# Performance work log

Hardware: AMD Instinct MI355X
Metric: run time of the kernel (lower is better)

## Reference

```python
import jax, jax.numpy as jnp
import numpy as np

HID = 128  # hidden_dim

def _run_layer(x, W, b):
    """x: [B,T,Cin,H,W]; W: [4*HID, Cin+HID] (gate order i,f,o,g); b: [4*HID]."""
    B, T, Cin, H, Wd = x.shape
    h0 = jnp.zeros((B, HID, H, Wd), x.dtype)
    c0 = jnp.zeros_like(h0)
    xt = jnp.moveaxis(x, 1, 0)  # [T,B,Cin,H,W]

    def step(carry, x_t):
        h, c = carry
        z = jnp.concatenate([x_t, h], axis=1)                     # [B,Cin+HID,H,W]
        gates = jnp.einsum('bchw,gc->bghw', z, W) + b[None, :, None, None]
        i, f, o, g = jnp.split(gates, 4, axis=1)                  # each [B,HID,H,W]
        c_n = jax.nn.sigmoid(f) * c + jax.nn.sigmoid(i) * jnp.tanh(g)
        h_n = jax.nn.sigmoid(o) * jnp.tanh(c_n)
        return (h_n, c_n), h_n

    (hT, cT), hs = jax.lax.scan(step, (h0, c0), xt)
    return jnp.moveaxis(hs, 0, 1), hT, cT  # [B,T,HID,H,W], [B,HID,H,W] x2


def setup_inputs() -> dict:
    key = jax.random.key(0)
    ks = jax.random.split(key, 5)
    B, T, Cin, H, W = 8, 32, 64, 32, 32
    x = jax.random.normal(ks[0], (B, T, Cin, H, W), dtype=jnp.float32)
    W0 = jax.random.normal(ks[1], (4 * HID, Cin + HID), dtype=jnp.float32) * 0.05
    b0 = jax.random.normal(ks[2], (4 * HID,), dtype=jnp.float32) * 0.05
    W1 = jax.random.normal(ks[3], (4 * HID, HID + HID), dtype=jnp.float32) * 0.05
    b1 = jax.random.normal(ks[4], (4 * HID,), dtype=jnp.float32) * 0.05
    return {"x": x, "W0": W0, "b0": b0, "W1": W1, "b1": b1}


def reference(x, W0, b0, W1, b1):
    y0, _, _ = _run_layer(x, W0, b0)      # layer 0
    y1, hT, cT = _run_layer(y0, W1, b1)   # layer 1 (last layer)
    return y1, hT, cT
```

## Files before the change

kernel.cpp:

```cpp
#include <hip/hip_runtime.h>

typedef short bf16x8 __attribute__((ext_vector_type(8)));
typedef short bf16x4 __attribute__((ext_vector_type(4)));
typedef float f32x4  __attribute__((ext_vector_type(4)));

#define HID 128
#define TT 32
#define HWSZ 1024
#define PX 32
#define NTHREADS 512

__device__ __forceinline__ float bf2f(unsigned short u) {
    union { unsigned int i; float f; } v; v.i = ((unsigned int)u) << 16; return v.f;
}
__device__ __forceinline__ unsigned short f2bf(float f) {
    union { float f; unsigned int i; } v; v.f = f;
    unsigned int u = v.i;
    return (unsigned short)((u + 0x7fffu + ((u >> 16) & 1u)) >> 16);
}
__device__ __forceinline__ float frcp(float x) { return __builtin_amdgcn_rcpf(x); }
__device__ __forceinline__ float sigm(float x) { return frcp(1.0f + __expf(-x)); }
__device__ __forceinline__ float ftanh(float x){ return 1.0f - 2.0f * frcp(1.0f + __expf(2.0f * x)); }

template <int CIN, bool FINAL, bool IN_LOCAL, bool OUT_LOCAL>
__global__ __launch_bounds__(NTHREADS, 2)
void lstm_layer(const void* __restrict__ in_, const float* __restrict__ W,
                const float* __restrict__ bias, void* __restrict__ y_,
                float* __restrict__ hT, float* __restrict__ cT)
{
    constexpr int K      = CIN + HID;
    constexpr int XK     = CIN / 32;
    constexpr int KITERS = K / 32;
    constexpr int XB0 = 0, XB1 = CIN, HB0 = 2 * CIN, HB1 = 2 * CIN + HID;
    constexpr int PITCH = 2 * CIN + 2 * HID + 8;
    constexpr int NIT = (PX * CIN / 4) / NTHREADS;

    const float* inF          = (const float*)in_;
    const unsigned short* inL = (const unsigned short*)in_;
    float* yF                 = (float*)y_;
    unsigned short* yL        = (unsigned short*)y_;

    __shared__ __align__(16) unsigned short z[PX][PITCH];

    const int tid  = threadIdx.x;
    const int wave = tid >> 6;
    const int lane = tid & 63;
    const int q    = lane >> 4;
    const int ln   = lane & 15;

    const int p0  = blockIdx.x * PX;
    const int b   = p0 >> 10;
    const int hw0 = p0 & 1023;

    const long long locbase = (long long)blockIdx.x * TT * PX * HID;
    const long long inFbase = (long long)b * TT * CIN * HWSZ + hw0;

    bf16x8 Af[KITERS][4];
    #pragma unroll
    for (int k = 0; k < KITERS; ++k) {
        #pragma unroll
        for (int g = 0; g < 4; ++g) {
            const float* wp = W + (g * HID + wave * 16 + ln) * K + k * 32 + q * 8;
            bf16x8 v;
            #pragma unroll
            for (int j = 0; j < 8; ++j) v[j] = (short)f2bf(wp[j]);
            Af[k][g] = v;
        }
    }
    f32x4 bs[4];
    #pragma unroll
    for (int g = 0; g < 4; ++g)
        bs[g] = *(const f32x4*)(bias + g * HID + wave * 16 + q * 4);

    const int ch0 = wave * 16 + q * 4;

    #pragma unroll
    for (int idx = tid; idx < PX * HID; idx += NTHREADS)
        z[idx & (PX - 1)][HB0 + (idx >> 5)] = 0;
    if (IN_LOCAL) {
        bf16x8 v = *(const bf16x8*)(inL + locbase + tid * 8);
        *(bf16x8*)&z[tid >> 4][XB0 + (tid & 15) * 8] = v;
    } else {
        #pragma unroll
        for (int it = 0; it < NIT; ++it) {
            const int idx = tid + it * NTHREADS;
            const int px = idx & 31, c0 = (idx >> 5) * 4;
            bf16x4 v;
            #pragma unroll
            for (int j = 0; j < 4; ++j) v[j] = (short)f2bf(inF[inFbase + (c0 + j) * HWSZ + px]);
            *(bf16x4*)&z[px][XB0 + c0] = v;
        }
    }
    __syncthreads();

    float cst[2][4];
    #pragma unroll
    for (int mt = 0; mt < 2; ++mt)
        #pragma unroll
        for (int r = 0; r < 4; ++r) cst[mt][r] = 0.0f;

    #pragma unroll 2
    for (int t = 0; t < TT; ++t) {
        const int cur = t & 1;
        const int xb_r = cur ? XB1 : XB0, xb_w = cur ? XB0 : XB1;
        const int hb_r = cur ? HB1 : HB0, hb_w = cur ? HB0 : HB1;
        const int tn = (t + 1 < TT) ? (t + 1) : t;

        bf16x8 pfv;
        float pff[NIT][4];
        if (IN_LOCAL) {
            pfv = *(const bf16x8*)(inL + locbase + (long long)tn * PX * HID + tid * 8);
        } else {
            #pragma unroll
            for (int it = 0; it < NIT; ++it) {
                const int idx = tid + it * NTHREADS;
                const int px = idx & 31, c0 = (idx >> 5) * 4;
                #pragma unroll
                for (int j = 0; j < 4; ++j)
                    pff[it][j] = inF[inFbase + (long long)tn * CIN * HWSZ + (c0 + j) * HWSZ + px];
            }
        }

        f32x4 acc[2][4];
        #pragma unroll
        for (int mt = 0; mt < 2; ++mt)
            #pragma unroll
            for (int g = 0; g < 4; ++g) acc[mt][g] = (f32x4){0.f, 0.f, 0.f, 0.f};

        #pragma unroll
        for (int k = 0; k < KITERS; ++k) {
            const int koff = (k < XK) ? (xb_r + k * 32) : (hb_r + (k - XK) * 32);
            const bf16x8 p0v = *(const bf16x8*)&z[ln][koff + q * 8];
            const bf16x8 p1v = *(const bf16x8*)&z[16 + ln][koff + q * 8];
            #pragma unroll
            for (int g = 0; g < 4; ++g) {
                acc[0][g] = __builtin_amdgcn_mfma_f32_16x16x32_bf16(Af[k][g], p0v, acc[0][g], 0, 0, 0);
                acc[1][g] = __builtin_amdgcn_mfma_f32_16x16x32_bf16(Af[k][g], p1v, acc[1][g], 0, 0, 0);
            }
        }

        #pragma unroll
        for (int mt = 0; mt < 2; ++mt) {
            const int px = mt * 16 + ln;
            bf16x4 hv;
            #pragma unroll
            for (int r = 0; r < 4; ++r) {
                const float iv = sigm(acc[mt][0][r] + bs[0][r]);
                const float fv = sigm(acc[mt][1][r] + bs[1][r]);
                const float ov = sigm(acc[mt][2][r] + bs[2][r]);
                const float gv = ftanh(acc[mt][3][r] + bs[3][r]);
                const float c  = fv * cst[mt][r] + iv * gv;
                cst[mt][r] = c;
                const float h = ov * ftanh(c);
                hv[r] = (short)f2bf(h);
                if (FINAL && t == TT - 1)
                    cT[(b * HID + ch0 + r) * HWSZ + hw0 + px] = c;
            }
            *(bf16x4*)&z[px][hb_w + ch0] = hv;
        }

        if (IN_LOCAL) {
            *(bf16x8*)&z[tid >> 4][xb_w + (tid & 15) * 8] = pfv;
        } else {
            #pragma unroll
            for (int it = 0; it < NIT; ++it) {
                const int idx = tid + it * NTHREADS;
                const int px = idx & 31, c0 = (idx >> 5) * 4;
                bf16x4 v;
                #pragma unroll
                for (int j = 0; j < 4; ++j) v[j] = (short)f2bf(pff[it][j]);
                *(bf16x4*)&z[px][xb_w + c0] = v;
            }
        }

        __syncthreads();

        if (FINAL || !OUT_LOCAL) {
            const int c = tid >> 2, px8 = (tid & 3) * 8;
            float f[8];
            #pragma unroll
            for (int j = 0; j < 8; ++j) f[j] = bf2f(z[px8 + j][hb_w + c]);
            float* yp = yF + (long long)(b * TT + t) * HID * HWSZ + c * HWSZ + hw0 + px8;
            *(f32x4*)yp       = (f32x4){f[0], f[1], f[2], f[3]};
            *(f32x4*)(yp + 4) = (f32x4){f[4], f[5], f[6], f[7]};
            if (FINAL && t == TT - 1) {
                float* hp = hT + (long long)(b * HID + c) * HWSZ + hw0 + px8;
                *(f32x4*)hp       = (f32x4){f[0], f[1], f[2], f[3]};
                *(f32x4*)(hp + 4) = (f32x4){f[4], f[5], f[6], f[7]};
            }
        } else {
            bf16x8 v = *(const bf16x8*)&z[tid >> 4][hb_w + (tid & 15) * 8];
            *(bf16x8*)(yL + locbase + (long long)t * PX * HID + tid * 8) = v;
        }
    }
}

extern "C" void kernel_launch(void* const* d_in, const int* in_sizes, int n_in,
                              void* d_out, int out_size, void* d_ws, size_t ws_size,
                              hipStream_t stream) {
    const float* x  = (const float*)d_in[0];
    const float* W0 = (const float*)d_in[1];
    const float* b0 = (const float*)d_in[2];
    const float* W1 = (const float*)d_in[3];
    const float* b1 = (const float*)d_in[4];
    float* out = (float*)d_out;

    float* y  = out;
    float* hT = out + 33554432;
    float* cT = out + 34603008;

    dim3 grid(8192 / PX), block(NTHREADS);

    const size_t y0_bytes = (size_t)8 * HWSZ * TT * HID * 2;
    if (ws_size >= y0_bytes) {
        unsigned short* y0 = (unsigned short*)d_ws;
        lstm_layer<64,  false, false, true ><<<grid, block, 0, stream>>>(x,  W0, b0, y0, nullptr, nullptr);
        lstm_layer<128, true,  true,  false><<<grid, block, 0, stream>>>(y0, W1, b1, y,  hT, cT);
    } else {
        lstm_layer<64,  false, false, false><<<grid, block, 0, stream>>>(x, W0, b0, y, nullptr, nullptr);
        lstm_layer<128, true,  false, false><<<grid, block, 0, stream>>>(y, W1, b1, y, hT, cT);
    }
}
```

Before: 355.3 us.

## Software-pipeline input projection one step ahead and write y directly from registers

Restructures the recurrent loop so the input-to-gate MFMA for step t+1 runs during step t, after the recurrent h MFMAs. This takes the x-part of the GEMM off the serial dependency chain. A three-slot x ring buffer in LDS with prefetch two steps ahead supports this, and the bias is folded into the accumulator init. The fp32 y/hT outputs are now stored straight from registers instead of going through an LDS round trip after the barrier. The change also uses the v_cvt_pk_bf16_f32 instruction for packed conversion and replaces __syncthreads with a raw s_barrier, at the cost of more accumulator registers and less coalesced 4-byte strided global stores.

```diff
diff --git a/kernel.cpp b/kernel.cpp
--- a/kernel.cpp
+++ b/kernel.cpp
@@ -3,6 +3,7 @@
 typedef short bf16x8 __attribute__((ext_vector_type(8)));
 typedef short bf16x4 __attribute__((ext_vector_type(4)));
 typedef float f32x4  __attribute__((ext_vector_type(4)));
+typedef unsigned int u32x2 __attribute__((ext_vector_type(2)));
 
 #define HID 128
 #define TT 32
@@ -10,13 +11,15 @@
 #define PX 32
 #define NTHREADS 512
 
-__device__ __forceinline__ float bf2f(unsigned short u) {
-    union { unsigned int i; float f; } v; v.i = ((unsigned int)u) << 16; return v.f;
-}
 __device__ __forceinline__ unsigned short f2bf(float f) {
     union { float f; unsigned int i; } v; v.f = f;
     unsigned int u = v.i;
     return (unsigned short)((u + 0x7fffu + ((u >> 16) & 1u)) >> 16);
+}
+__device__ __forceinline__ unsigned int cvt_pk_bf16(float lo, float hi) {
+    unsigned int r;
+    asm("v_cvt_pk_bf16_f32 %0, %1, %2" : "=v"(r) : "v"(lo), "v"(hi));
+    return r;
 }
 __device__ __forceinline__ float frcp(float x) { return __builtin_amdgcn_rcpf(x); }
 __device__ __forceinline__ float sigm(float x) { return frcp(1.0f + __expf(-x)); }
@@ -30,9 +33,10 @@
 {
     constexpr int K      = CIN + HID;
     constexpr int XK     = CIN / 32;
+    constexpr int HK     = HID / 32;
     constexpr int KITERS = K / 32;
-    constexpr int XB0 = 0, XB1 = CIN, HB0 = 2 * CIN, HB1 = 2 * CIN + HID;
-    constexpr int PITCH = 2 * CIN + 2 * HID + 8;
+    constexpr int HB0 = 3 * CIN, HB1 = 3 * CIN + HID;
+    constexpr int PITCH = 3 * CIN + 2 * HID + 8;
     constexpr int NIT = (PX * CIN / 4) / NTHREADS;
 
     const float* inF          = (const float*)in_;
@@ -73,22 +77,31 @@
         bs[g] = *(const f32x4*)(bias + g * HID + wave * 16 + q * 4);
 
     const int ch0 = wave * 16 + q * 4;
+    float* const ybase = yF + ((long long)b * TT * HID + ch0) * HWSZ + hw0;
 
     #pragma unroll
     for (int idx = tid; idx < PX * HID; idx += NTHREADS)
         z[idx & (PX - 1)][HB0 + (idx >> 5)] = 0;
     if (IN_LOCAL) {
-        bf16x8 v = *(const bf16x8*)(inL + locbase + tid * 8);
-        *(bf16x8*)&z[tid >> 4][XB0 + (tid & 15) * 8] = v;
+        bf16x8 v0 = *(const bf16x8*)(inL + locbase + tid * 8);
+        bf16x8 v1 = *(const bf16x8*)(inL + locbase + (long long)PX * HID + tid * 8);
+        *(bf16x8*)&z[tid >> 4][(tid & 15) * 8] = v0;
+        *(bf16x8*)&z[tid >> 4][CIN + (tid & 15) * 8] = v1;
     } else {
         #pragma unroll
         for (int it = 0; it < NIT; ++it) {
             const int idx = tid + it * NTHREADS;
-            const int px = idx & 31, c0 = (idx >> 5) * 4;
-            bf16x4 v;
+            const int pxs = idx & 31, c0 = (idx >> 5) * 4;
+            float a0[4], a1[4];
             #pragma unroll
-            for (int j = 0; j < 4; ++j) v[j] = (short)f2bf(inF[inFbase + (c0 + j) * HWSZ + px]);
-            *(bf16x4*)&z[px][XB0 + c0] = v;
+            for (int j = 0; j < 4; ++j) a0[j] = inF[inFbase + (c0 + j) * HWSZ + pxs];
+            #pragma unroll
+            for (int j = 0; j < 4; ++j) a1[j] = inF[inFbase + (long long)CIN * HWSZ + (c0 + j) * HWSZ + pxs];
+            u32x2 v0, v1;
+            v0[0] = cvt_pk_bf16(a0[0], a0[1]); v0[1] = cvt_pk_bf16(a0[2], a0[3]);
+            v1[0] = cvt_pk_bf16(a1[0], a1[1]); v1[1] = cvt_pk_bf16(a1[2], a1[3]);
+            *(u32x2*)&z[pxs][c0] = v0;
+            *(u32x2*)&z[pxs][CIN + c0] = v1;
         }
     }
     __syncthreads();
@@ -99,100 +112,121 @@
         #pragma unroll
         for (int r = 0; r < 4; ++r) cst[mt][r] = 0.0f;
 
-    #pragma unroll 2
-    for (int t = 0; t < TT; ++t) {
-        const int cur = t & 1;
-        const int xb_r = cur ? XB1 : XB0, xb_w = cur ? XB0 : XB1;
-        const int hb_r = cur ? HB1 : HB0, hb_w = cur ? HB0 : HB1;
-        const int tn = (t + 1 < TT) ? (t + 1) : t;
-
-        bf16x8 pfv;
-        float pff[NIT][4];
-        if (IN_LOCAL) {
-            pfv = *(const bf16x8*)(inL + locbase + (long long)tn * PX * HID + tid * 8);
-        } else {
-            #pragma unroll
-            for (int it = 0; it < NIT; ++it) {
-                const int idx = tid + it * NTHREADS;
-                const int px = idx & 31, c0 = (idx >> 5) * 4;
-                #pragma unroll
-                for (int j = 0; j < 4; ++j)
-                    pff[it][j] = inF[inFbase + (long long)tn * CIN * HWSZ + (c0 + j) * HWSZ + px];
-            }
+    f32x4 accA[2][4], accB[2][4];
+    #pragma unroll
+    for (int g = 0; g < 4; ++g) { accA[0][g] = bs[g]; accA[1][g] = bs[g]; }
+    #pragma unroll
+    for (int k = 0; k < XK; ++k) {
+        const int koff = k * 32;
+        const bf16x8 pv0 = *(const bf16x8*)&z[ln][koff + q * 8];
+        const bf16x8 pv1 = *(const bf16x8*)&z[16 + ln][koff + q * 8];
+        #pragma unroll
+        for (int g = 0; g < 4; ++g) {
+            accA[0][g] = __builtin_amdgcn_mfma_f32_16x16x32_bf16(Af[k][g], pv0, accA[0][g], 0, 0, 0);
+            accA[1][g] = __builtin_amdgcn_mfma_f32_16x16x32_bf16(Af[k][g], pv1, accA[1][g], 0, 0, 0);
         }
-
-        f32x4 acc[2][4];
-        #pragma unroll
-        for (int mt = 0; mt < 2; ++mt)
-            #pragma unroll
-            for (int g = 0; g < 4; ++g) acc[mt][g] = (f32x4){0.f, 0.f, 0.f, 0.f};
-
-        #pragma unroll
-        for (int k = 0; k < KITERS; ++k) {
-            const int koff = (k < XK) ? (xb_r + k * 32) : (hb_r + (k - XK) * 32);
-            const bf16x8 p0v = *(const bf16x8*)&z[ln][koff + q * 8];
-            const bf16x8 p1v = *(const bf16x8*)&z[16 + ln][koff + q * 8];
-            #pragma unroll
-            for (int g = 0; g < 4; ++g) {
-                acc[0][g] = __builtin_amdgcn_mfma_f32_16x16x32_bf16(Af[k][g], p0v, acc[0][g], 0, 0, 0);
-                acc[1][g] = __builtin_amdgcn_mfma_f32_16x16x32_bf16(Af[k][g], p1v, acc[1][g], 0, 0, 0);
-            }
-        }
-
-        #pragma unroll
-        for (int mt = 0; mt < 2; ++mt) {
-            const int px = mt * 16 + ln;
-            bf16x4 hv;
-            #pragma unroll
-            for (int r = 0; r < 4; ++r) {
-                const float iv = sigm(acc[mt][0][r] + bs[0][r]);
-                const float fv = sigm(acc[mt][1][r] + bs[1][r]);
-                const float ov = sigm(acc[mt][2][r] + bs[2][r]);
-                const float gv = ftanh(acc[mt][3][r] + bs[3][r]);
-                const float c  = fv * cst[mt][r] + iv * gv;
-                cst[mt][r] = c;
-                const float h = ov * ftanh(c);
-                hv[r] = (short)f2bf(h);
-                if (FINAL && t == TT - 1)
-                    cT[(b * HID + ch0 + r) * HWSZ + hw0 + px] = c;
-            }
-            *(bf16x4*)&z[px][hb_w + ch0] = hv;
-        }
-
-        if (IN_LOCAL) {
-            *(bf16x8*)&z[tid >> 4][xb_w + (tid & 15) * 8] = pfv;
-        } else {
-            #pragma unroll
-            for (int it = 0; it < NIT; ++it) {
-                const int idx = tid + it * NTHREADS;
-                const int px = idx & 31, c0 = (idx >> 5) * 4;
-                bf16x4 v;
-                #pragma unroll
-                for (int j = 0; j < 4; ++j) v[j] = (short)f2bf(pff[it][j]);
-                *(bf16x4*)&z[px][xb_w + c0] = v;
-            }
-        }
-
-        __syncthreads();
-
-        if (FINAL || !OUT_LOCAL) {
-            const int c = tid >> 2, px8 = (tid & 3) * 8;
-            float f[8];
-            #pragma unroll
-            for (int j = 0; j < 8; ++j) f[j] = bf2f(z[px8 + j][hb_w + c]);
-            float* yp = yF + (long long)(b * TT + t) * HID * HWSZ + c * HWSZ + hw0 + px8;
-            *(f32x4*)yp       = (f32x4){f[0], f[1], f[2], f[3]};
-            *(f32x4*)(yp + 4) = (f32x4){f[4], f[5], f[6], f[7]};
-            if (FINAL && t == TT - 1) {
-                float* hp = hT + (long long)(b * HID + c) * HWSZ + hw0 + px8;
-                *(f32x4*)hp       = (f32x4){f[0], f[1], f[2], f[3]};
-                *(f32x4*)(hp + 4) = (f32x4){f[4], f[5], f[6], f[7]};
-            }
-        } else {
-            bf16x8 v = *(const bf16x8*)&z[tid >> 4][hb_w + (tid & 15) * 8];
-            *(bf16x8*)(yL + locbase + (long long)t * PX * HID + tid * 8) = v;
-        }
-    }
+    }
+
+#define LSTM_STEP(T, PAR, ACCC, ACCN)                                            \
+    {                                                                            \
+        const int hb_r = (PAR) ? HB1 : HB0;                                      \
+        const int hb_w = (PAR) ? HB0 : HB1;                                      \
+        const int xs_n = ((T) + 1) % 3;                                          \
+        const int xs_w = ((T) + 2) % 3;                                          \
+        const int tn2  = ((T) + 2 < TT) ? (T) + 2 : TT - 1;                      \
+        bf16x8 pfv; float pff[NIT][4];                                           \
+        if (IN_LOCAL) {                                                          \
+            pfv = *(const bf16x8*)(inL + locbase + (long long)tn2 * PX * HID + tid * 8); \
+        } else {                                                                 \
+            _Pragma("unroll")                                                    \
+            for (int it = 0; it < NIT; ++it) {                                   \
+                const int idx = tid + it * NTHREADS;                             \
+                const int pxs = idx & 31, c0 = (idx >> 5) * 4;                   \
+                _Pragma("unroll")                                                \
+                for (int j = 0; j < 4; ++j)                                      \
+                    pff[it][j] = inF[inFbase + (long long)tn2 * CIN * HWSZ + (c0 + j) * HWSZ + pxs]; \
+            }                                                                    \
+        }                                                                        \
+        _Pragma("unroll")                                                        \
+        for (int k = 0; k < HK; ++k) {                                           \
+            const int koff = hb_r + k * 32;                                      \
+            const bf16x8 pv0 = *(const bf16x8*)&z[ln][koff + q * 8];             \
+            const bf16x8 pv1 = *(const bf16x8*)&z[16 + ln][koff + q * 8];        \
+            _Pragma("unroll")                                                    \
+            for (int g = 0; g < 4; ++g) {                                        \
+                ACCC[0][g] = __builtin_amdgcn_mfma_f32_16x16x32_bf16(Af[XK + k][g], pv0, ACCC[0][g], 0, 0, 0); \
+                ACCC[1][g] = __builtin_amdgcn_mfma_f32_16x16x32_bf16(Af[XK + k][g], pv1, ACCC[1][g], 0, 0, 0); \
+            }                                                                    \
+        }                                                                        \
+        _Pragma("unroll")                                                        \
+        for (int g = 0; g < 4; ++g) { ACCN[0][g] = bs[g]; ACCN[1][g] = bs[g]; }  \
+        _Pragma("unroll")                                                        \
+        for (int k = 0; k < XK; ++k) {                                           \
+            const int koff = xs_n * CIN + k * 32;                                \
+            const bf16x8 pv0 = *(const bf16x8*)&z[ln][koff + q * 8];             \
+            const bf16x8 pv1 = *(const bf16x8*)&z[16 + ln][koff + q * 8];        \
+            _Pragma("unroll")                                                    \
+            for (int g = 0; g < 4; ++g) {                                        \
+                ACCN[0][g] = __builtin_amdgcn_mfma_f32_16x16x32_bf16(Af[k][g], pv0, ACCN[0][g], 0, 0, 0); \
+                ACCN[1][g] = __builtin_amdgcn_mfma_f32_16x16x32_bf16(Af[k][g], pv1, ACCN[1][g], 0, 0, 0); \
+            }                                                                    \
+        }                                                                        \
+        _Pragma("unroll")                                                        \
+        for (int mt = 0; mt < 2; ++mt) {                                         \
+            const int px = mt * 16 + ln;                                         \
+            float hr[4];                                                         \
+            _Pragma("unroll")                                                    \
+            for (int r = 0; r < 4; ++r) {                                        \
+                const float iv = sigm(ACCC[mt][0][r]);                           \
+                const float fv = sigm(ACCC[mt][1][r]);                           \
+                const float ov = sigm(ACCC[mt][2][r]);                           \
+                const float gv = ftanh(ACCC[mt][3][r]);                          \
+                const float c  = fv * cst[mt][r] + iv * gv;                      \
+                cst[mt][r] = c;                                                  \
+                hr[r] = ov * ftanh(c);                                           \
+                if (FINAL && (T) == TT - 1)                                      \
+                    cT[((long long)(b * HID + ch0 + r)) * HWSZ + hw0 + px] = c;  \
+            }                                                                    \
+            u32x2 hv;                                                            \
+            hv[0] = cvt_pk_bf16(hr[0], hr[1]);                                   \
+            hv[1] = cvt_pk_bf16(hr[2], hr[3]);                                   \
+            *(u32x2*)&z[px][hb_w + ch0] = hv;                                    \
+            if (FINAL || !OUT_LOCAL) {                                           \
+                float* yp = ybase + (long long)(T) * (HID * HWSZ) + px;          \
+                yp[0] = hr[0]; yp[HWSZ] = hr[1];                                 \
+                yp[2 * HWSZ] = hr[2]; yp[3 * HWSZ] = hr[3];                      \
+                if (FINAL && (T) == TT - 1) {                                    \
+                    float* hp = hT + ((long long)(b * HID + ch0)) * HWSZ + hw0 + px; \
+                    hp[0] = hr[0]; hp[HWSZ] = hr[1];                             \
+                    hp[2 * HWSZ] = hr[2]; hp[3 * HWSZ] = hr[3];                  \
+                }                                                                \
+            }                                                                    \
+        }                                                                        \
+        if (IN_LOCAL) {                                                          \
+            *(bf16x8*)&z[tid >> 4][xs_w * CIN + (tid & 15) * 8] = pfv;           \
+        } else {                                                                 \
+            _Pragma("unroll")                                                    \
+            for (int it = 0; it < NIT; ++it) {                                   \
+                const int idx = tid + it * NTHREADS;                             \
+                const int pxs = idx & 31, c0 = (idx >> 5) * 4;                   \
+                u32x2 xv;                                                        \
+                xv[0] = cvt_pk_bf16(pff[it][0], pff[it][1]);                     \
+                xv[1] = cvt_pk_bf16(pff[it][2], pff[it][3]);                     \
+                *(u32x2*)&z[pxs][xs_w * CIN + c0] = xv;                          \
+            }                                                                    \
+        }                                                                        \
+        asm volatile("s_waitcnt lgkmcnt(0)\n\ts_barrier" ::: "memory");          \
+        if (!FINAL && OUT_LOCAL) {                                               \
+            bf16x8 hv8 = *(const bf16x8*)&z[tid >> 4][hb_w + (tid & 15) * 8];    \
+            *(bf16x8*)(yL + locbase + (long long)(T) * PX * HID + tid * 8) = hv8; \
+        }                                                                        \
+    }
+
+    for (int t = 0; t < TT; t += 2) {
+        LSTM_STEP(t,     0, accA, accB)
+        LSTM_STEP(t + 1, 1, accB, accA)
+    }
+#undef LSTM_STEP
 }
 
 extern "C" void kernel_launch(void* const* d_in, const int* in_sizes, int n_in,
```

New measurement: 364.6 us. 2.6% more time.

## Split LSTM block into input-projection and recurrent warp groups with LDS handoff

Applied to the files above, without the earlier changes.

Doubles the block to 1024 threads. Eight waves compute the input projection W_x·x_{t+1} plus bias one step ahead and hand it off through LDS accumulators, while the other eight waves do only the recurrent W_h·h GEMM and the gate math. This takes the input GEMM and the global x prefetch off the serial critical path of the recurrence. Other changes: output is written directly from registers without a transposing LDS pass, LDS reads use XOR swizzling, and bf16 packing uses v_cvt_pk_bf16_f32. The cost is two barriers per step across 16 waves, plus an fp32 accumulator exchange through LDS, with added risk to occupancy and register pressure.

```diff
diff --git a/kernel.cpp b/kernel.cpp
--- a/kernel.cpp
+++ b/kernel.cpp
@@ -1,52 +1,58 @@
 #include <hip/hip_runtime.h>
 
 typedef short bf16x8 __attribute__((ext_vector_type(8)));
-typedef short bf16x4 __attribute__((ext_vector_type(4)));
 typedef float f32x4  __attribute__((ext_vector_type(4)));
+typedef unsigned int u32x2 __attribute__((ext_vector_type(2)));
 
 #define HID 128
 #define TT 32
 #define HWSZ 1024
 #define PX 32
-#define NTHREADS 512
-
-__device__ __forceinline__ float bf2f(unsigned short u) {
-    union { unsigned int i; float f; } v; v.i = ((unsigned int)u) << 16; return v.f;
-}
+#define NTHREADS 1024
+
 __device__ __forceinline__ unsigned short f2bf(float f) {
     union { float f; unsigned int i; } v; v.f = f;
     unsigned int u = v.i;
     return (unsigned short)((u + 0x7fffu + ((u >> 16) & 1u)) >> 16);
 }
+__device__ __forceinline__ unsigned int cvt_pk_bf16(float lo, float hi) {
+    unsigned int r;
+    asm("v_cvt_pk_bf16_f32 %0, %1, %2" : "=v"(r) : "v"(lo), "v"(hi));
+    return r;
+}
 __device__ __forceinline__ float frcp(float x) { return __builtin_amdgcn_rcpf(x); }
 __device__ __forceinline__ float sigm(float x) { return frcp(1.0f + __expf(-x)); }
 __device__ __forceinline__ float ftanh(float x){ return 1.0f - 2.0f * frcp(1.0f + __expf(2.0f * x)); }
 
+#define BAR() asm volatile("s_waitcnt lgkmcnt(0)\n\ts_barrier" ::: "memory")
+
 template <int CIN, bool FINAL, bool IN_LOCAL, bool OUT_LOCAL>
-__global__ __launch_bounds__(NTHREADS, 2)
+__global__ __launch_bounds__(NTHREADS, 4)
 void lstm_layer(const void* __restrict__ in_, const float* __restrict__ W,
                 const float* __restrict__ bias, void* __restrict__ y_,
                 float* __restrict__ hT, float* __restrict__ cT)
 {
-    constexpr int K      = CIN + HID;
-    constexpr int XK     = CIN / 32;
-    constexpr int KITERS = K / 32;
-    constexpr int XB0 = 0, XB1 = CIN, HB0 = 2 * CIN, HB1 = 2 * CIN + HID;
-    constexpr int PITCH = 2 * CIN + 2 * HID + 8;
-    constexpr int NIT = (PX * CIN / 4) / NTHREADS;
+    constexpr int XK  = CIN / 32;
+    constexpr int HK  = HID / 32;
+    constexpr int NIT = (PX * CIN / 4) / 512;
 
     const float* inF          = (const float*)in_;
     const unsigned short* inL = (const unsigned short*)in_;
     float* yF                 = (float*)y_;
     unsigned short* yL        = (unsigned short*)y_;
 
-    __shared__ __align__(16) unsigned short z[PX][PITCH];
+    __shared__ __align__(16) float          accS[8 * 2 * 4 * 256];
+    __shared__ __align__(16) unsigned short hS[2][PX][HID];
+    __shared__ __align__(16) unsigned short xS[2][PX][CIN];
+    __shared__ __align__(16) float          biasS[4 * HID];
 
     const int tid  = threadIdx.x;
     const int wave = tid >> 6;
     const int lane = tid & 63;
     const int q    = lane >> 4;
     const int ln   = lane & 15;
+    const bool isB = wave < 8;
+    const int  wp  = wave & 7;
 
     const int p0  = blockIdx.x * PX;
     const int b   = p0 >> 10;
@@ -55,142 +61,217 @@
     const long long locbase = (long long)blockIdx.x * TT * PX * HID;
     const long long inFbase = (long long)b * TT * CIN * HWSZ + hw0;
 
-    bf16x8 Af[KITERS][4];
-    #pragma unroll
-    for (int k = 0; k < KITERS; ++k) {
-        #pragma unroll
-        for (int g = 0; g < 4; ++g) {
-            const float* wp = W + (g * HID + wave * 16 + ln) * K + k * 32 + q * 8;
-            bf16x8 v;
-            #pragma unroll
-            for (int j = 0; j < 8; ++j) v[j] = (short)f2bf(wp[j]);
-            Af[k][g] = v;
-        }
-    }
-    f32x4 bs[4];
-    #pragma unroll
-    for (int g = 0; g < 4; ++g)
-        bs[g] = *(const f32x4*)(bias + g * HID + wave * 16 + q * 4);
-
-    const int ch0 = wave * 16 + q * 4;
-
-    #pragma unroll
-    for (int idx = tid; idx < PX * HID; idx += NTHREADS)
-        z[idx & (PX - 1)][HB0 + (idx >> 5)] = 0;
-    if (IN_LOCAL) {
-        bf16x8 v = *(const bf16x8*)(inL + locbase + tid * 8);
-        *(bf16x8*)&z[tid >> 4][XB0 + (tid & 15) * 8] = v;
-    } else {
-        #pragma unroll
-        for (int it = 0; it < NIT; ++it) {
-            const int idx = tid + it * NTHREADS;
-            const int px = idx & 31, c0 = (idx >> 5) * 4;
-            bf16x4 v;
-            #pragma unroll
-            for (int j = 0; j < 4; ++j) v[j] = (short)f2bf(inF[inFbase + (c0 + j) * HWSZ + px]);
-            *(bf16x4*)&z[px][XB0 + c0] = v;
+    if (tid < HID) *(f32x4*)&biasS[tid * 4] = *(const f32x4*)&bias[tid * 4];
+    *(u32x2*)&hS[0][tid >> 5][(tid & 31) * 4] = (u32x2){0u, 0u};
+    {
+        const int t0   = isB ? 0 : 1;
+        const int tid2 = isB ? tid : tid - 512;
+        if (IN_LOCAL) {
+            bf16x8 v = *(const bf16x8*)(inL + locbase + (long long)t0 * PX * HID + tid2 * 8);
+            const int px = tid2 >> 4, c8 = (tid2 & 15) * 8;
+            *(bf16x8*)&xS[t0][px][c8 ^ ((px & 7) << 3)] = v;
+        } else {
+            #pragma unroll
+            for (int it = 0; it < NIT; ++it) {
+                const int idx = tid2 + it * 512;
+                const int px = idx & 31, c0 = (idx >> 5) * 4;
+                float a[4];
+                #pragma unroll
+                for (int j = 0; j < 4; ++j)
+                    a[j] = inF[inFbase + (long long)t0 * CIN * HWSZ + (c0 + j) * HWSZ + px];
+                u32x2 v;
+                v[0] = cvt_pk_bf16(a[0], a[1]); v[1] = cvt_pk_bf16(a[2], a[3]);
+                *(u32x2*)&xS[t0][px][c0 ^ ((px & 7) << 3)] = v;
+            }
         }
     }
     __syncthreads();
 
-    float cst[2][4];
-    #pragma unroll
-    for (int mt = 0; mt < 2; ++mt)
+    if (isB) {
+        bf16x8 AfB[HK][4];
         #pragma unroll
-        for (int r = 0; r < 4; ++r) cst[mt][r] = 0.0f;
-
-    #pragma unroll 2
-    for (int t = 0; t < TT; ++t) {
-        const int cur = t & 1;
-        const int xb_r = cur ? XB1 : XB0, xb_w = cur ? XB0 : XB1;
-        const int hb_r = cur ? HB1 : HB0, hb_w = cur ? HB0 : HB1;
-        const int tn = (t + 1 < TT) ? (t + 1) : t;
-
-        bf16x8 pfv;
-        float pff[NIT][4];
-        if (IN_LOCAL) {
-            pfv = *(const bf16x8*)(inL + locbase + (long long)tn * PX * HID + tid * 8);
-        } else {
-            #pragma unroll
-            for (int it = 0; it < NIT; ++it) {
-                const int idx = tid + it * NTHREADS;
-                const int px = idx & 31, c0 = (idx >> 5) * 4;
-                #pragma unroll
-                for (int j = 0; j < 4; ++j)
-                    pff[it][j] = inF[inFbase + (long long)tn * CIN * HWSZ + (c0 + j) * HWSZ + px];
-            }
-        }
-
-        f32x4 acc[2][4];
+        for (int k = 0; k < HK; ++k)
+            #pragma unroll
+            for (int g = 0; g < 4; ++g) {
+                const float* wptr = W + (g * HID + wp * 16 + ln) * (CIN + HID) + CIN + k * 32 + q * 8;
+                bf16x8 v;
+                #pragma unroll
+                for (int j = 0; j < 8; ++j) v[j] = (short)f2bf(wptr[j]);
+                AfB[k][g] = v;
+            }
+        const int ch0 = wp * 16 + q * 4;
+        float cst[2][4];
         #pragma unroll
         for (int mt = 0; mt < 2; ++mt)
             #pragma unroll
-            for (int g = 0; g < 4; ++g) acc[mt][g] = (f32x4){0.f, 0.f, 0.f, 0.f};
-
+            for (int r = 0; r < 4; ++r) cst[mt][r] = 0.0f;
+        float* const ybase = yF + ((long long)b * TT * HID + ch0) * HWSZ + hw0;
+
+        BAR();
+        #pragma unroll 2
+        for (int t = 0; t < TT; ++t) {
+            f32x4 acc[2][4];
+            #pragma unroll
+            for (int mt = 0; mt < 2; ++mt)
+                #pragma unroll
+                for (int g = 0; g < 4; ++g)
+                    acc[mt][g] = *(const f32x4*)&accS[(((wp * 2 + mt) * 4 + g) * 64 + lane) * 4];
+            BAR();
+            const unsigned short (*hR)[HID] = hS[t & 1];
+            #pragma unroll
+            for (int k = 0; k < HK; ++k) {
+                const int ofs = (k * 32 + q * 8) ^ ((ln & 7) << 3);
+                const bf16x8 p0v = *(const bf16x8*)&hR[ln][ofs];
+                const bf16x8 p1v = *(const bf16x8*)&hR[16 + ln][ofs];
+                #pragma unroll
+                for (int g = 0; g < 4; ++g) {
+                    acc[0][g] = __builtin_amdgcn_mfma_f32_16x16x32_bf16(AfB[k][g], p0v, acc[0][g], 0, 0, 0);
+                    acc[1][g] = __builtin_amdgcn_mfma_f32_16x16x32_bf16(AfB[k][g], p1v, acc[1][g], 0, 0, 0);
+                }
+            }
+            #pragma unroll
+            for (int mt = 0; mt < 2; ++mt) {
+                const int px = mt * 16 + ln;
+                float hr[4];
+                #pragma unroll
+                for (int r = 0; r < 4; ++r) {
+                    const float iv = sigm(acc[mt][0][r]);
+                    const float fv = sigm(acc[mt][1][r]);
+                    const float ov = sigm(acc[mt][2][r]);
+                    const float gv = ftanh(acc[mt][3][r]);
+                    const float c  = fv * cst[mt][r] + iv * gv;
+                    cst[mt][r] = c;
+                    hr[r] = ov * ftanh(c);
+                    if (FINAL && t == TT - 1)
+                        cT[((long long)(b * HID + ch0 + r)) * HWSZ + hw0 + px] = c;
+                }
+                u32x2 hv;
+                hv[0] = cvt_pk_bf16(hr[0], hr[1]);
+                hv[1] = cvt_pk_bf16(hr[2], hr[3]);
+                *(u32x2*)&hS[(t + 1) & 1][px][ch0 ^ ((px & 7) << 3)] = hv;
+                if (FINAL || !OUT_LOCAL) {
+                    float* yp = ybase + (long long)t * (HID * HWSZ) + px;
+                    yp[0] = hr[0]; yp[HWSZ] = hr[1];
+                    yp[2 * HWSZ] = hr[2]; yp[3 * HWSZ] = hr[3];
+                    if (FINAL && t == TT - 1) {
+                        float* hp = hT + ((long long)(b * HID + ch0)) * HWSZ + hw0 + px;
+                        hp[0] = hr[0]; hp[HWSZ] = hr[1];
+                        hp[2 * HWSZ] = hr[2]; hp[3 * HWSZ] = hr[3];
+                    }
+                } else {
+                    *(u32x2*)(yL + locbase + ((long long)t * PX + px) * HID + ch0) = hv;
+                }
+            }
+            BAR();
+        }
+    } else {
+        bf16x8 AfA[XK][4];
         #pragma unroll
-        for (int k = 0; k < KITERS; ++k) {
-            const int koff = (k < XK) ? (xb_r + k * 32) : (hb_r + (k - XK) * 32);
-            const bf16x8 p0v = *(const bf16x8*)&z[ln][koff + q * 8];
-            const bf16x8 p1v = *(const bf16x8*)&z[16 + ln][koff + q * 8];
+        for (int k = 0; k < XK; ++k)
             #pragma unroll
             for (int g = 0; g < 4; ++g) {
-                acc[0][g] = __builtin_amdgcn_mfma_f32_16x16x32_bf16(Af[k][g], p0v, acc[0][g], 0, 0, 0);
-                acc[1][g] = __builtin_amdgcn_mfma_f32_16x16x32_bf16(Af[k][g], p1v, acc[1][g], 0, 0, 0);
-            }
-        }
-
-        #pragma unroll
-        for (int mt = 0; mt < 2; ++mt) {
-            const int px = mt * 16 + ln;
-            bf16x4 hv;
-            #pragma unroll
-            for (int r = 0; r < 4; ++r) {
-                const float iv = sigm(acc[mt][0][r] + bs[0][r]);
-                const float fv = sigm(acc[mt][1][r] + bs[1][r]);
-                const float ov = sigm(acc[mt][2][r] + bs[2][r]);
-                const float gv = ftanh(acc[mt][3][r] + bs[3][r]);
-                const float c  = fv * cst[mt][r] + iv * gv;
-                cst[mt][r] = c;
-                const float h = ov * ftanh(c);
-                hv[r] = (short)f2bf(h);
-                if (FINAL && t == TT - 1)
-                    cT[(b * HID + ch0 + r) * HWSZ + hw0 + px] = c;
-            }
-            *(bf16x4*)&z[px][hb_w + ch0] = hv;
-        }
-
+                const float* wptr = W + (g * HID + wp * 16 + ln) * (CIN + HID) + k * 32 + q * 8;
+                bf16x8 v;
+                #pragma unroll
+                for (int j = 0; j < 8; ++j) v[j] = (short)f2bf(wptr[j]);
+                AfA[k][g] = v;
+            }
+        const int tid2 = tid - 512;
+        bf16x8 xreg8;
+        float pff[NIT][4];
+
+        {
+            f32x4 acc[2][4];
+            #pragma unroll
+            for (int g = 0; g < 4; ++g) {
+                const f32x4 bf = *(const f32x4*)&biasS[g * HID + wp * 16 + q * 4];
+                acc[0][g] = bf; acc[1][g] = bf;
+            }
+            #pragma unroll
+            for (int k = 0; k < XK; ++k) {
+                const int ofs = (k * 32 + q * 8) ^ ((ln & 7) << 3);
+                const bf16x8 p0v = *(const bf16x8*)&xS[0][ln][ofs];
+                const bf16x8 p1v = *(const bf16x8*)&xS[0][16 + ln][ofs];
+                #pragma unroll
+                for (int g = 0; g < 4; ++g) {
+                    acc[0][g] = __builtin_amdgcn_mfma_f32_16x16x32_bf16(AfA[k][g], p0v, acc[0][g], 0, 0, 0);
+                    acc[1][g] = __builtin_amdgcn_mfma_f32_16x16x32_bf16(AfA[k][g], p1v, acc[1][g], 0, 0, 0);
+                }
+            }
+            #pragma unroll
+            for (int mt = 0; mt < 2; ++mt)
+                #pragma unroll
+                for (int g = 0; g < 4; ++g)
+                    *(f32x4*)&accS[(((wp * 2 + mt) * 4 + g) * 64 + lane) * 4] = acc[mt][g];
+        }
         if (IN_LOCAL) {
-            *(bf16x8*)&z[tid >> 4][xb_w + (tid & 15) * 8] = pfv;
+            xreg8 = *(const bf16x8*)(inL + locbase + (long long)2 * PX * HID + tid2 * 8);
         } else {
             #pragma unroll
             for (int it = 0; it < NIT; ++it) {
-                const int idx = tid + it * NTHREADS;
+                const int idx = tid2 + it * 512;
                 const int px = idx & 31, c0 = (idx >> 5) * 4;
-                bf16x4 v;
-                #pragma unroll
-                for (int j = 0; j < 4; ++j) v[j] = (short)f2bf(pff[it][j]);
-                *(bf16x4*)&z[px][xb_w + c0] = v;
-            }
-        }
-
-        __syncthreads();
-
-        if (FINAL || !OUT_LOCAL) {
-            const int c = tid >> 2, px8 = (tid & 3) * 8;
-            float f[8];
-            #pragma unroll
-            for (int j = 0; j < 8; ++j) f[j] = bf2f(z[px8 + j][hb_w + c]);
-            float* yp = yF + (long long)(b * TT + t) * HID * HWSZ + c * HWSZ + hw0 + px8;
-            *(f32x4*)yp       = (f32x4){f[0], f[1], f[2], f[3]};
-            *(f32x4*)(yp + 4) = (f32x4){f[4], f[5], f[6], f[7]};
-            if (FINAL && t == TT - 1) {
-                float* hp = hT + (long long)(b * HID + c) * HWSZ + hw0 + px8;
-                *(f32x4*)hp       = (f32x4){f[0], f[1], f[2], f[3]};
-                *(f32x4*)(hp + 4) = (f32x4){f[4], f[5], f[6], f[7]};
-            }
-        } else {
-            bf16x8 v = *(const bf16x8*)&z[tid >> 4][hb_w + (tid & 15) * 8];
-            *(bf16x8*)(yL + locbase + (long long)t * PX * HID + tid * 8) = v;
+                #pragma unroll
+                for (int j = 0; j < 4; ++j)
+                    pff[it][j] = inF[inFbase + (long long)2 * CIN * HWSZ + (c0 + j) * HWSZ + px];
+            }
+        }
+        BAR();
+
+        #pragma unroll 2
+        for (int t = 0; t < TT; ++t) {
+            BAR();
+            f32x4 acc[2][4];
+            #pragma unroll
+            for (int g = 0; g < 4; ++g) {
+                const f32x4 bf = *(const f32x4*)&biasS[g * HID + wp * 16 + q * 4];
+                acc[0][g] = bf; acc[1][g] = bf;
+            }
+            const unsigned short (*xR)[CIN] = xS[(t + 1) & 1];
+            #pragma unroll
+            for (int k = 0; k < XK; ++k) {
+                const int ofs = (k * 32 + q * 8) ^ ((ln & 7) << 3);
+                const bf16x8 p0v = *(const bf16x8*)&xR[ln][ofs];
+                const bf16x8 p1v = *(const bf16x8*)&xR[16 + ln][ofs];
+                #pragma unroll
+                for (int g = 0; g < 4; ++g) {
+                    acc[0][g] = __builtin_amdgcn_mfma_f32_16x16x32_bf16(AfA[k][g], p0v, acc[0][g], 0, 0, 0);
+                    acc[1][g] = __builtin_amdgcn_mfma_f32_16x16x32_bf16(AfA[k][g], p1v, acc[1][g], 0, 0, 0);
+                }
+            }
+            #pragma unroll
+            for (int mt = 0; mt < 2; ++mt)
+                #pragma unroll
+                for (int g = 0; g < 4; ++g)
+                    *(f32x4*)&accS[(((wp * 2 + mt) * 4 + g) * 64 + lane) * 4] = acc[mt][g];
+            if (IN_LOCAL) {
+                const int px = tid2 >> 4, c8 = (tid2 & 15) * 8;
+                *(bf16x8*)&xS[t & 1][px][c8 ^ ((px & 7) << 3)] = xreg8;
+            } else {
+                #pragma unroll
+                for (int it = 0; it < NIT; ++it) {
+                    const int idx = tid2 + it * 512;
+                    const int px = idx & 31, c0 = (idx >> 5) * 4;
+                    u32x2 v;
+                    v[0] = cvt_pk_bf16(pff[it][0], pff[it][1]);
+                    v[1] = cvt_pk_bf16(pff[it][2], pff[it][3]);
+                    *(u32x2*)&xS[t & 1][px][c0 ^ ((px & 7) << 3)] = v;
+                }
+            }
+            const int tn = (t + 3 < TT) ? t + 3 : TT - 1;
+            if (IN_LOCAL) {
+                xreg8 = *(const bf16x8*)(inL + locbase + (long long)tn * PX * HID + tid2 * 8);
+            } else {
+                #pragma unroll
+                for (int it = 0; it < NIT; ++it) {
+                    const int idx = tid2 + it * 512;
+                    const int px = idx & 31, c0 = (idx >> 5) * 4;
+                    #pragma unroll
+                    for (int j = 0; j < 4; ++j)
+                        pff[it][j] = inF[inFbase + (long long)tn * CIN * HWSZ + (c0 + j) * HWSZ + px];
+                }
+            }
+            BAR();
         }
     }
 }
```

After: 411.4 us. 1.16x slower.

## Double waves per block with gate-interleaved MFMA rows and fused gate math

Applied to the files above, without the earlier changes.

Raises the block to 1024 threads so each wave owns 8 channels. Weight rows are interleaved so the four gates of one channel land in one accumulator vector, and the bias is folded into the accumulator start. Gate math is rewritten to share reciprocals, packed bf16 conversion is used, and fp32 outputs are written straight from registers, dropping the LDS round trip. A lighter barrier and s_setprio around the epilogue are added, at the cost of narrower, less coalesced global stores and higher register pressure at 1024 threads.

```diff
diff --git a/kernel.cpp b/kernel.cpp
--- a/kernel.cpp
+++ b/kernel.cpp
@@ -3,37 +3,41 @@
 typedef short bf16x8 __attribute__((ext_vector_type(8)));
 typedef short bf16x4 __attribute__((ext_vector_type(4)));
 typedef float f32x4  __attribute__((ext_vector_type(4)));
+typedef unsigned int u32x2 __attribute__((ext_vector_type(2)));
 
 #define HID 128
 #define TT 32
 #define HWSZ 1024
 #define PX 32
-#define NTHREADS 512
-
-__device__ __forceinline__ float bf2f(unsigned short u) {
-    union { unsigned int i; float f; } v; v.i = ((unsigned int)u) << 16; return v.f;
-}
+#define NTHREADS 1024
+
 __device__ __forceinline__ unsigned short f2bf(float f) {
     union { float f; unsigned int i; } v; v.f = f;
     unsigned int u = v.i;
     return (unsigned short)((u + 0x7fffu + ((u >> 16) & 1u)) >> 16);
 }
+__device__ __forceinline__ unsigned int cvt_pk_bf16(float lo, float hi) {
+    unsigned int r;
+    asm("v_cvt_pk_bf16_f32 %0, %1, %2" : "=v"(r) : "v"(lo), "v"(hi));
+    return r;
+}
 __device__ __forceinline__ float frcp(float x) { return __builtin_amdgcn_rcpf(x); }
-__device__ __forceinline__ float sigm(float x) { return frcp(1.0f + __expf(-x)); }
-__device__ __forceinline__ float ftanh(float x){ return 1.0f - 2.0f * frcp(1.0f + __expf(2.0f * x)); }
+
+#define BARRIER() asm volatile("s_waitcnt lgkmcnt(0)\n\ts_barrier" ::: "memory")
 
 template <int CIN, bool FINAL, bool IN_LOCAL, bool OUT_LOCAL>
-__global__ __launch_bounds__(NTHREADS, 2)
+__global__ __launch_bounds__(NTHREADS, 4)
 void lstm_layer(const void* __restrict__ in_, const float* __restrict__ W,
                 const float* __restrict__ bias, void* __restrict__ y_,
                 float* __restrict__ hT, float* __restrict__ cT)
 {
     constexpr int K      = CIN + HID;
     constexpr int XK     = CIN / 32;
-    constexpr int KITERS = K / 32;
-    constexpr int XB0 = 0, XB1 = CIN, HB0 = 2 * CIN, HB1 = 2 * CIN + HID;
-    constexpr int PITCH = 2 * CIN + 2 * HID + 8;
-    constexpr int NIT = (PX * CIN / 4) / NTHREADS;
+    constexpr int HK     = HID / 32;
+    constexpr int KITERS = XK + HK;
+    constexpr int HB     = 2 * CIN;
+    constexpr int PITCH  = 2 * CIN + 2 * HID + 8;
+    constexpr int NIT2   = CIN / 64;
 
     const float* inF          = (const float*)in_;
     const unsigned short* inL = (const unsigned short*)in_;
@@ -55,142 +59,147 @@
     const long long locbase = (long long)blockIdx.x * TT * PX * HID;
     const long long inFbase = (long long)b * TT * CIN * HWSZ + hw0;
 
-    bf16x8 Af[KITERS][4];
+    const int chb = wave * 8;
+    const int chq = chb + q;
+
+    bf16x8 Af[KITERS][2];
     #pragma unroll
     for (int k = 0; k < KITERS; ++k) {
         #pragma unroll
-        for (int g = 0; g < 4; ++g) {
-            const float* wp = W + (g * HID + wave * 16 + ln) * K + k * 32 + q * 8;
+        for (int tau = 0; tau < 2; ++tau) {
+            const float* wp = W + ((ln & 3) * HID + chb + tau * 4 + (ln >> 2)) * K + k * 32 + q * 8;
             bf16x8 v;
             #pragma unroll
             for (int j = 0; j < 8; ++j) v[j] = (short)f2bf(wp[j]);
-            Af[k][g] = v;
-        }
-    }
-    f32x4 bs[4];
+            Af[k][tau] = v;
+        }
+    }
+    f32x4 bsv[2];
     #pragma unroll
-    for (int g = 0; g < 4; ++g)
-        bs[g] = *(const f32x4*)(bias + g * HID + wave * 16 + q * 4);
-
-    const int ch0 = wave * 16 + q * 4;
-
-    #pragma unroll
-    for (int idx = tid; idx < PX * HID; idx += NTHREADS)
-        z[idx & (PX - 1)][HB0 + (idx >> 5)] = 0;
+    for (int tau = 0; tau < 2; ++tau)
+        #pragma unroll
+        for (int r = 0; r < 4; ++r)
+            bsv[tau][r] = bias[r * HID + chq + tau * 4];
+
+    float* const ybase = yF + ((long long)b * TT * HID) * HWSZ + hw0;
+
+    *(u32x2*)&z[tid >> 5][HB + (tid & 31) * 4] = (u32x2){0u, 0u};
     if (IN_LOCAL) {
-        bf16x8 v = *(const bf16x8*)(inL + locbase + tid * 8);
-        *(bf16x8*)&z[tid >> 4][XB0 + (tid & 15) * 8] = v;
+        bf16x4 v = *(const bf16x4*)(inL + locbase + tid * 4);
+        *(bf16x4*)&z[tid >> 5][(tid & 31) * 4] = v;
     } else {
         #pragma unroll
-        for (int it = 0; it < NIT; ++it) {
+        for (int it = 0; it < NIT2; ++it) {
             const int idx = tid + it * NTHREADS;
-            const int px = idx & 31, c0 = (idx >> 5) * 4;
-            bf16x4 v;
-            #pragma unroll
-            for (int j = 0; j < 4; ++j) v[j] = (short)f2bf(inF[inFbase + (c0 + j) * HWSZ + px]);
-            *(bf16x4*)&z[px][XB0 + c0] = v;
+            const int pxs = idx & 31, c0 = (idx >> 5) * 2;
+            const float a0 = inF[inFbase + (c0 + 0) * HWSZ + pxs];
+            const float a1 = inF[inFbase + (c0 + 1) * HWSZ + pxs];
+            *(unsigned int*)&z[pxs][c0] = cvt_pk_bf16(a0, a1);
         }
     }
     __syncthreads();
 
-    float cst[2][4];
+    float cst[2][2];
     #pragma unroll
     for (int mt = 0; mt < 2; ++mt)
         #pragma unroll
-        for (int r = 0; r < 4; ++r) cst[mt][r] = 0.0f;
+        for (int tau = 0; tau < 2; ++tau) cst[mt][tau] = 0.0f;
 
     #pragma unroll 2
     for (int t = 0; t < TT; ++t) {
-        const int cur = t & 1;
-        const int xb_r = cur ? XB1 : XB0, xb_w = cur ? XB0 : XB1;
-        const int hb_r = cur ? HB1 : HB0, hb_w = cur ? HB0 : HB1;
-        const int tn = (t + 1 < TT) ? (t + 1) : t;
-
-        bf16x8 pfv;
-        float pff[NIT][4];
+        const int cur = t & 1, nxt = cur ^ 1;
+        const int tn = (t + 1 < TT) ? t + 1 : TT - 1;
+
+        bf16x4 pfv;
+        float pf[NIT2][2];
         if (IN_LOCAL) {
-            pfv = *(const bf16x8*)(inL + locbase + (long long)tn * PX * HID + tid * 8);
+            pfv = *(const bf16x4*)(inL + locbase + (long long)tn * PX * HID + tid * 4);
         } else {
             #pragma unroll
-            for (int it = 0; it < NIT; ++it) {
+            for (int it = 0; it < NIT2; ++it) {
                 const int idx = tid + it * NTHREADS;
-                const int px = idx & 31, c0 = (idx >> 5) * 4;
-                #pragma unroll
-                for (int j = 0; j < 4; ++j)
-                    pff[it][j] = inF[inFbase + (long long)tn * CIN * HWSZ + (c0 + j) * HWSZ + px];
+                const int pxs = idx & 31, c0 = (idx >> 5) * 2;
+                pf[it][0] = inF[inFbase + (long long)tn * CIN * HWSZ + (c0 + 0) * HWSZ + pxs];
+                pf[it][1] = inF[inFbase + (long long)tn * CIN * HWSZ + (c0 + 1) * HWSZ + pxs];
             }
         }
 
-        f32x4 acc[2][4];
+        f32x4 acc[2][2];
         #pragma unroll
         for (int mt = 0; mt < 2; ++mt)
             #pragma unroll
-            for (int g = 0; g < 4; ++g) acc[mt][g] = (f32x4){0.f, 0.f, 0.f, 0.f};
-
-        #pragma unroll
-        for (int k = 0; k < KITERS; ++k) {
-            const int koff = (k < XK) ? (xb_r + k * 32) : (hb_r + (k - XK) * 32);
-            const bf16x8 p0v = *(const bf16x8*)&z[ln][koff + q * 8];
-            const bf16x8 p1v = *(const bf16x8*)&z[16 + ln][koff + q * 8];
-            #pragma unroll
-            for (int g = 0; g < 4; ++g) {
-                acc[0][g] = __builtin_amdgcn_mfma_f32_16x16x32_bf16(Af[k][g], p0v, acc[0][g], 0, 0, 0);
-                acc[1][g] = __builtin_amdgcn_mfma_f32_16x16x32_bf16(Af[k][g], p1v, acc[1][g], 0, 0, 0);
-            }
-        }
-
+            for (int tau = 0; tau < 2; ++tau) acc[mt][tau] = bsv[tau];
+
+        #pragma unroll
+        for (int k = 0; k < XK; ++k) {
+            const int koff = cur * CIN + k * 32 + q * 8;
+            const bf16x8 pv0 = *(const bf16x8*)&z[ln][koff];
+            const bf16x8 pv1 = *(const bf16x8*)&z[16 + ln][koff];
+            acc[0][0] = __builtin_amdgcn_mfma_f32_16x16x32_bf16(Af[k][0], pv0, acc[0][0], 0, 0, 0);
+            acc[0][1] = __builtin_amdgcn_mfma_f32_16x16x32_bf16(Af[k][1], pv0, acc[0][1], 0, 0, 0);
+            acc[1][0] = __builtin_amdgcn_mfma_f32_16x16x32_bf16(Af[k][0], pv1, acc[1][0], 0, 0, 0);
+            acc[1][1] = __builtin_amdgcn_mfma_f32_16x16x32_bf16(Af[k][1], pv1, acc[1][1], 0, 0, 0);
+        }
+        #pragma unroll
+        for (int k = 0; k < HK; ++k) {
+            const int koff = HB + cur * HID + k * 32 + q * 8;
+            const bf16x8 pv0 = *(const bf16x8*)&z[ln][koff];
+            const bf16x8 pv1 = *(const bf16x8*)&z[16 + ln][koff];
+            acc[0][0] = __builtin_amdgcn_mfma_f32_16x16x32_bf16(Af[XK + k][0], pv0, acc[0][0], 0, 0, 0);
+            acc[0][1] = __builtin_amdgcn_mfma_f32_16x16x32_bf16(Af[XK + k][1], pv0, acc[0][1], 0, 0, 0);
+            acc[1][0] = __builtin_amdgcn_mfma_f32_16x16x32_bf16(Af[XK + k][0], pv1, acc[1][0], 0, 0, 0);
+            acc[1][1] = __builtin_amdgcn_mfma_f32_16x16x32_bf16(Af[XK + k][1], pv1, acc[1][1], 0, 0, 0);
+        }
+
+        __builtin_amdgcn_s_setprio(1);
         #pragma unroll
         for (int mt = 0; mt < 2; ++mt) {
             const int px = mt * 16 + ln;
-            bf16x4 hv;
-            #pragma unroll
-            for (int r = 0; r < 4; ++r) {
-                const float iv = sigm(acc[mt][0][r] + bs[0][r]);
-                const float fv = sigm(acc[mt][1][r] + bs[1][r]);
-                const float ov = sigm(acc[mt][2][r] + bs[2][r]);
-                const float gv = ftanh(acc[mt][3][r] + bs[3][r]);
-                const float c  = fv * cst[mt][r] + iv * gv;
-                cst[mt][r] = c;
-                const float h = ov * ftanh(c);
-                hv[r] = (short)f2bf(h);
-                if (FINAL && t == TT - 1)
-                    cT[(b * HID + ch0 + r) * HWSZ + hw0 + px] = c;
+            #pragma unroll
+            for (int tau = 0; tau < 2; ++tau) {
+                const int ch = chq + tau * 4;
+                const float ei = __expf(-acc[mt][tau][0]);
+                const float ef = __expf(-acc[mt][tau][1]);
+                const float eo = __expf(-acc[mt][tau][2]);
+                const float eg = __expf(-2.0f * acc[mt][tau][3]);
+                const float a1 = 1.0f + ei;
+                const float a2 = 1.0f + eg;
+                const float a3 = 1.0f + ef;
+                const float p12 = a1 * a2;
+                const float num = cst[mt][tau] * p12 + (1.0f - eg) * a3;
+                const float c   = num * frcp(a3 * p12);
+                cst[mt][tau] = c;
+                const float ec = __expf(-2.0f * c);
+                const float h  = (1.0f - ec) * frcp((1.0f + eo) * (1.0f + ec));
+
+                z[px][HB + nxt * HID + ch] = f2bf(h);
+                if (FINAL || !OUT_LOCAL) {
+                    ybase[((long long)t * HID + ch) * HWSZ + px] = h;
+                    if (FINAL && t == TT - 1) {
+                        hT[((long long)(b * HID + ch)) * HWSZ + hw0 + px] = h;
+                        cT[((long long)(b * HID + ch)) * HWSZ + hw0 + px] = c;
+                    }
+                }
             }
-            *(bf16x4*)&z[px][hb_w + ch0] = hv;
-        }
+        }
+        __builtin_amdgcn_s_setprio(0);
 
         if (IN_LOCAL) {
-            *(bf16x8*)&z[tid >> 4][xb_w + (tid & 15) * 8] = pfv;
+            *(bf16x4*)&z[tid >> 5][nxt * CIN + (tid & 31) * 4] = pfv;
         } else {
             #pragma unroll
-            for (int it = 0; it < NIT; ++it) {
+            for (int it = 0; it < NIT2; ++it) {
                 const int idx = tid + it * NTHREADS;
-                const int px = idx & 31, c0 = (idx >> 5) * 4;
-                bf16x4 v;
-                #pragma unroll
-                for (int j = 0; j < 4; ++j) v[j] = (short)f2bf(pff[it][j]);
-                *(bf16x4*)&z[px][xb_w + c0] = v;
+                const int pxs = idx & 31, c0 = (idx >> 5) * 2;
+                *(unsigned int*)&z[pxs][nxt * CIN + c0] = cvt_pk_bf16(pf[it][0], pf[it][1]);
             }
         }
 
-        __syncthreads();
-
-        if (FINAL || !OUT_LOCAL) {
-            const int c = tid >> 2, px8 = (tid & 3) * 8;
-            float f[8];
-            #pragma unroll
-            for (int j = 0; j < 8; ++j) f[j] = bf2f(z[px8 + j][hb_w + c]);
-            float* yp = yF + (long long)(b * TT + t) * HID * HWSZ + c * HWSZ + hw0 + px8;
-            *(f32x4*)yp       = (f32x4){f[0], f[1], f[2], f[3]};
-            *(f32x4*)(yp + 4) = (f32x4){f[4], f[5], f[6], f[7]};
-            if (FINAL && t == TT - 1) {
-                float* hp = hT + (long long)(b * HID + c) * HWSZ + hw0 + px8;
-                *(f32x4*)hp       = (f32x4){f[0], f[1], f[2], f[3]};
-                *(f32x4*)(hp + 4) = (f32x4){f[4], f[5], f[6], f[7]};
-            }
-        } else {
-            bf16x8 v = *(const bf16x8*)&z[tid >> 4][hb_w + (tid & 15) * 8];
-            *(bf16x8*)(yL + locbase + (long long)t * PX * HID + tid * 8) = v;
+        BARRIER();
+
+        if (!FINAL && OUT_LOCAL) {
+            bf16x4 hv = *(const bf16x4*)&z[tid >> 5][HB + nxt * HID + (tid & 31) * 4];
+            *(bf16x4*)(yL + locbase + (long long)t * PX * HID + tid * 4) = hv;
         }
     }
 }
```

Measured after the change: 350.9 us. Within noise of the previous version (-1.2%).
